# Optimization experiments

Measured on AMD Instinct MI355X. Metric: run time of the kernel, lower is better.

## Reference

```python
import jax, jax.numpy as jnp
import numpy as np

B, S, I, C, N, V, O = 32, 256, 256, 512, 1024, 64, 256
EPS = 1e-12


def setup_inputs() -> dict:
    key = jax.random.key(0)
    ks = iter(jax.random.split(key, 40))

    def rn(shape, scale=0.05):
        return (jax.random.normal(next(ks), shape, jnp.float32) * scale)

    inp = {
        'x': jax.random.normal(next(ks), (B, S, I), jnp.float32),
        # LSTM controller (PyTorch gate order i,f,g,o)
        'lstm_Wih': rn((4 * C, I + V)), 'lstm_Whh': rn((4 * C, C)),
        'lstm_bih': rn((4 * C,)), 'lstm_bhh': rn((4 * C,)),
        # read head
        'r_key_W': rn((V, C)), 'r_key_b': rn((V,)),
        'r_str_W': rn((1, C)), 'r_str_b': rn((1,)),
        'r_gate_W': rn((1, C)), 'r_gate_b': rn((1,)),
        'r_shift_W': rn((3, C)), 'r_shift_b': rn((3,)),
        'r_gamma_W': rn((1, C)), 'r_gamma_b': rn((1,)),
        # write head (uses its own key/strength layers, plus erase/add)
        'w_key_W': rn((V, C)), 'w_key_b': rn((V,)),
        'w_str_W': rn((1, C)), 'w_str_b': rn((1,)),
        'w_erase_W': rn((V, C)), 'w_erase_b': rn((V,)),
        'w_add_W': rn((V, C)), 'w_add_b': rn((V,)),
        # output projection
        'out_W': rn((O, C + V)), 'out_b': rn((O,)),
    }
    return inp


def _lin(x, W, b):
    return x @ W.T + b


def _normalize(x, axis):
    n = jnp.linalg.norm(x, axis=axis, keepdims=True)
    return x / jnp.maximum(n, EPS)


def _content_addressing(key_vec, memory, strength):
    # key_vec: [B,V], memory: [B,N,V], strength: [B,1]
    kn = _normalize(key_vec, 1)
    mn = _normalize(memory, 2)
    sim = jnp.einsum('bv,bnv->bn', kn, mn)
    return jax.nn.softmax(strength * sim, axis=1)


def _ntm_forward(x, lstm_Wih, lstm_Whh, lstm_bih, lstm_bhh,
                 r_key_W, r_key_b, r_str_W, r_str_b, r_gate_W, r_gate_b,
                 r_shift_W, r_shift_b, r_gamma_W, r_gamma_b,
                 w_key_W, w_key_b, w_str_W, w_str_b,
                 w_erase_W, w_erase_b, w_add_W, w_add_b, out_W, out_b):
    b = x.shape[0]
    h0 = jnp.zeros((b, C), x.dtype)
    c0 = jnp.zeros((b, C), x.dtype)
    mem0 = jnp.zeros((b, N, V), x.dtype)
    rv0 = jnp.zeros((b, V), x.dtype)

    def step(carry, xt):
        h, c, memory, read_vec = carry
        # LSTM cell
        ci = jnp.concatenate([xt, read_vec], axis=1)          # [B, I+V]
        gates = _lin(ci, lstm_Wih, lstm_bih) + _lin(h, lstm_Whh, lstm_bhh)
        ig, fg, gg, og = jnp.split(gates, 4, axis=1)
        c = jax.nn.sigmoid(fg) * c + jax.nn.sigmoid(ig) * jnp.tanh(gg)
        h = jax.nn.sigmoid(og) * jnp.tanh(c)

        # read head
        key_r = jnp.tanh(_lin(h, r_key_W, r_key_b))
        str_r = jax.nn.softplus(_lin(h, r_str_W, r_str_b))
        gate = jax.nn.sigmoid(_lin(h, r_gate_W, r_gate_b))
        _shift = jax.nn.softmax(_lin(h, r_shift_W, r_shift_b), axis=1)  # computed but unused (as in source)
        gamma = 1.0 + jax.nn.softplus(_lin(h, r_gamma_W, r_gamma_b))
        cw = _content_addressing(key_r, memory, str_r)        # [B,N]
        sharp = cw ** gamma
        lw = sharp / jnp.sum(sharp, axis=1, keepdims=True)
        fw = gate * lw + (1.0 - gate) * cw
        read_vec = jnp.einsum('bn,bnv->bv', fw, memory)

        # write head (erase then add)
        key_w = jnp.tanh(_lin(h, w_key_W, w_key_b))
        str_w = jax.nn.softplus(_lin(h, w_str_W, w_str_b))
        ww = _content_addressing(key_w, memory, str_w)        # [B,N]
        erase = jax.nn.sigmoid(_lin(h, w_erase_W, w_erase_b))  # [B,V]
        add = jnp.tanh(_lin(h, w_add_W, w_add_b))              # [B,V]
        memory = memory * (1.0 - ww[:, :, None] * erase[:, None, :]) \
                 + ww[:, :, None] * add[:, None, :]

        out = _lin(jnp.concatenate([h, read_vec], axis=1), out_W, out_b)
        return (h, c, memory, read_vec), out

    (_, _, final_memory, _), outs = jax.lax.scan(
        step, (h0, c0, mem0, rv0), jnp.swapaxes(x, 0, 1))
    return jnp.swapaxes(outs, 0, 1), final_memory


def reference(x, lstm_Wih, lstm_Whh, lstm_bih, lstm_bhh,
              r_key_W, r_key_b, r_str_W, r_str_b, r_gate_W, r_gate_b,
              r_shift_W, r_shift_b, r_gamma_W, r_gamma_b,
              w_key_W, w_key_b, w_str_W, w_str_b,
              w_erase_W, w_erase_b, w_add_W, w_add_b, out_W, out_b):
    return _ntm_forward(x, lstm_Wih, lstm_Whh, lstm_bih, lstm_bhh,
                        r_key_W, r_key_b, r_str_W, r_str_b, r_gate_W, r_gate_b,
                        r_shift_W, r_shift_b, r_gamma_W, r_gamma_b,
                        w_key_W, w_key_b, w_str_W, w_str_b,
                        w_erase_W, w_erase_b, w_add_W, w_add_b, out_W, out_b)
```

## Files before the change

### kernel.cpp

```cpp
#include <hip/hip_runtime.h>

#define Bv 32
#define Sv 256
#define Iv 256
#define Cv 512
#define Nv 1024
#define Vv 64
#define Ov 256
#define NBLK 256
#define NTHR 256

#define CLAIM_I(x)   ((x)*8)
#define GAL_I(x,q)   (64 + ((x)*4+(q))*8)
#define XROOT_I(x)   (320 + (x)*8)
#define PB_I(x,b)    (384 + ((x)*4+(b))*8)
#define ZERO_BYTES   (640*4)
#define FBASE 1024
#define HBU(x,t1,bb)  (FBASE + (x)*2048 + (t1)*1024 + (bb)*256)
#define RVPU(x,bb,k)  (FBASE + 16384 + (x)*1024 + (bb)*256 + (k)*32)
#define SUMPF(x,bb,k) (FBASE + 24576 + (x)*128 + (bb)*32 + (k)*4)
#define HDSF(x,bb)    (FBASE + 25600 + ((x)*4+(bb))*260)

struct KP {
  const float *x, *Wih, *Whh, *bih, *bhh;
  const float *rkW, *rkb, *rsW, *rsb, *rgW, *rgb, *rgammaW, *rgammab;
  const float *wkW, *wkb, *wsW, *wsb, *weW, *web, *waW, *wab;
  const float *outW, *outb;
  float *out;
  float *memout;
  float *ws;
};

typedef _Float16 half2v __attribute__((ext_vector_type(2)));
union HU { unsigned u; half2v h; };

__device__ inline float sigf(float x){ return 1.f/(1.f+expf(-x)); }
__device__ inline float softplusf(float x){ return fmaxf(x,0.f) + log1pf(expf(-fabsf(x))); }
__device__ inline unsigned packh(float a, float b){
  HU z; z.h = half2v{(_Float16)a, (_Float16)b}; return z.u;
}
__device__ inline float h2lo(unsigned u){ HU z; z.u = u; return (float)z.h.x; }
__device__ inline float h2hi(unsigned u){ HU z; z.u = u; return (float)z.h.y; }
__device__ inline float dot2(unsigned w, unsigned a, float acc){
  HU wu, au; wu.u = w; au.u = a;
  return __builtin_amdgcn_fdot2(wu.h, au.h, acc, false);
}

__device__ inline void stg_f(float* p, float v){
  asm volatile("global_store_dword %0, %1, off sc0" :: "v"(p), "v"(v) : "memory");
}
__device__ inline void stg_u(unsigned* p, unsigned v){
  asm volatile("global_store_dword %0, %1, off sc0" :: "v"(p), "v"(v) : "memory");
}
#define LDG4U(dst, addr) asm volatile("global_load_dwordx4 %0, %1, off sc0" : "=v"(dst) : "v"(addr) : "memory")
#define LDG4F(dst, addr) asm volatile("global_load_dwordx4 %0, %1, off sc0" : "=v"(dst) : "v"(addr) : "memory")
#define LDGU(dst, addr)  asm volatile("global_load_dword %0, %1, off sc0"  : "=v"(dst) : "v"(addr) : "memory")
#define WAITV do { asm volatile("s_waitcnt vmcnt(0)" ::: "memory"); __builtin_amdgcn_sched_barrier(0); } while(0)

#define AADD(p,v) __hip_atomic_fetch_add((p),(v),__ATOMIC_RELAXED,__HIP_MEMORY_SCOPE_AGENT)
#define ALD(p)    __hip_atomic_load((p),__ATOMIC_RELAXED,__HIP_MEMORY_SCOPE_AGENT)

#define SPIN(cond_expr) do { unsigned sp = 0; \
  while (cond_expr){ __builtin_amdgcn_s_sleep(2); \
    if (((++sp)&1023u)==0u && (__builtin_amdgcn_s_memrealtime()-t0) > 300000000ULL) break; } } while(0)

__device__ inline float headact(int o, float s){
  if (o < 64)  return tanhf(s);
  if (o == 64) return softplusf(s);
  if (o == 65) return sigf(s);
  if (o == 66) return 1.f + softplusf(s);
  if (o < 131) return tanhf(s);
  if (o == 131) return softplusf(s);
  if (o < 196) return sigf(s);
  return tanhf(s);
}
__device__ inline void head_src(const KP& P, int o, const float** row, float* bias){
  if (o < 64)       { *row = P.rkW + o*Cv;        *bias = P.rkb[o]; }
  else if (o == 64) { *row = P.rsW;               *bias = P.rsb[0]; }
  else if (o == 65) { *row = P.rgW;               *bias = P.rgb[0]; }
  else if (o == 66) { *row = P.rgammaW;           *bias = P.rgammab[0]; }
  else if (o < 131) { *row = P.wkW + (o-67)*Cv;   *bias = P.wkb[o-67]; }
  else if (o == 131){ *row = P.wsW;               *bias = P.wsb[0]; }
  else if (o < 196) { *row = P.weW + (o-132)*Cv;  *bias = P.web[o-132]; }
  else              { *row = P.waW + (o-196)*Cv;  *bias = P.wab[o-196]; }
}

__global__ __launch_bounds__(NTHR) void ntm_kernel(KP P){
  __shared__ unsigned Wg[64][420];
  __shared__ unsigned actL[4][420];
  __shared__ float memL[128][66];
  __shared__ float gb[64][4];
  __shared__ float biasL[64];
  __shared__ float htmpf[16][5];
  __shared__ unsigned hOwnL[256];
  __shared__ float headsL[264];
  __shared__ float knr[64], knw[64];
  __shared__ float scal[8];
  __shared__ float fwL[128], wwL[128];
  __shared__ float red[32][9];
  __shared__ float red2[2][4];
  __shared__ float sumred[8][4];
  __shared__ float rvpartL[4][64];
  __shared__ float rvfin[64];
  __shared__ int sXcd, sRank;

  const int tid = threadIdx.x;
  float* wsf = P.ws;
  unsigned* wsu = (unsigned*)P.ws;
  int* wsi = (int*)P.ws;
  const unsigned long long t0 = __builtin_amdgcn_s_memrealtime();

  if (tid == 0){
    unsigned xcc;
    asm volatile("s_getreg_b32 %0, hwreg(20, 0, 32)" : "=s"(xcc));
    int xc = (int)(xcc & 7u);
    int rk = AADD(&wsi[CLAIM_I(xc)], 1);
    sXcd = xc; sRank = rk & 31;
  }
  __syncthreads();
  const int xcd = sXcd, rank = sRank;
  const int bl_own = rank >> 3;
  const int rk8 = rank & 7;
  const int bglob = xcd*4 + bl_own;
  const int obase = (rk8 < 4) ? rk8*33 : 132 + (rk8-4)*32;

  for (int idx = tid; idx < 64*416; idx += NTHR){
    int rl = idx / 416, u = idx % 416;
    int gr = (rl>>4)*Cv + rank*16 + (rl&15);
    int c0 = 2*u;
    float a, b2;
    if (c0 < 320){ a = P.Wih[gr*320 + c0]; b2 = P.Wih[gr*320 + c0 + 1]; }
    else { int q = c0 - 320; a = P.Whh[gr*512 + q]; b2 = P.Whh[gr*512 + q + 1]; }
    Wg[rl][u] = packh(a, b2);
  }
  if (tid < 64){
    int gr = (tid>>4)*Cv + rank*16 + (tid&15);
    biasL[tid] = P.bih[gr] + P.bhh[gr];
  }
  for (int idx = tid; idx < 128*66; idx += NTHR) ((float*)memL)[idx] = 0.f;
  __syncthreads();

  float cS = 0.f;
  float er = 0.f, eg = 0.f, ew = 0.f;
  int gs = 0, pbs = 0;

  for (int t = 0; t < Sv; ++t){
    {
      int bb = tid>>6, part = tid&63;
      const float* xp = P.x + ((size_t)(xcd*4+bb)*Sv + (size_t)t)*Iv + part*4;
      float4 xv = *(const float4*)xp;
      actL[bb][part*2]   = packh(xv.x, xv.y);
      actL[bb][part*2+1] = packh(xv.z, xv.w);
      if (t > 0){
        uint4 hq;
        LDG4U(hq, wsu + HBU(xcd,(t+1)&1,bb) + part*4);
        unsigned q0=0,q1=0,q2=0,q3=0,q4=0,q5=0,q6=0,q7=0;
        int b2 = tid>>5, uix = tid&31;
        if (tid < 128){
          const unsigned* rb = wsu + RVPU(xcd,b2,0) + uix;
          LDGU(q0, rb+0*32); LDGU(q1, rb+1*32); LDGU(q2, rb+2*32); LDGU(q3, rb+3*32);
          LDGU(q4, rb+4*32); LDGU(q5, rb+5*32); LDGU(q6, rb+6*32); LDGU(q7, rb+7*32);
        }
        WAITV;
        *(uint4*)&actL[bb][160 + part*4] = hq;
        if (tid < 128){
          float lo = h2lo(q0)+h2lo(q1)+h2lo(q2)+h2lo(q3)+h2lo(q4)+h2lo(q5)+h2lo(q6)+h2lo(q7);
          float hi = h2hi(q0)+h2hi(q1)+h2hi(q2)+h2hi(q3)+h2hi(q4)+h2hi(q5)+h2hi(q6)+h2hi(q7);
          actL[b2][128+uix] = packh(lo, hi);
        }
      } else {
        for (int idx = tid; idx < 4*288; idx += NTHR){
          int bb2 = idx/288, u = 128 + idx%288;
          actL[bb2][u] = 0u;
        }
      }
    }
    __syncthreads();
    {
      int g = tid>>6, l = tid&63, rr = l>>2, bb = l&3, row = g*16+rr;
      const unsigned* wr = &Wg[row][0];
      const unsigned* ar = &actL[bb][0];
      float a0 = biasL[row], a1 = 0.f, a2 = 0.f, a3 = 0.f;
      #pragma unroll 13
      for (int u = 0; u < 416; u += 8){
        uint4 w0 = *(const uint4*)(wr+u);
        uint4 v0 = *(const uint4*)(ar+u);
        uint4 w1 = *(const uint4*)(wr+u+4);
        uint4 v1 = *(const uint4*)(ar+u+4);
        a0 = dot2(w0.x, v0.x, a0); a1 = dot2(w0.y, v0.y, a1);
        a2 = dot2(w0.z, v0.z, a2); a3 = dot2(w0.w, v0.w, a3);
        a0 = dot2(w1.x, v1.x, a0); a1 = dot2(w1.y, v1.y, a1);
        a2 = dot2(w1.z, v1.z, a2); a3 = dot2(w1.w, v1.w, a3);
      }
      gb[row][bb] = (a0+a1)+(a2+a3);
    }
    __syncthreads();
    if (tid < 64){
      int j = tid>>2, bb = tid&3;
      float ig = gb[j][bb], fg = gb[16+j][bb], gg = gb[32+j][bb], og = gb[48+j][bb];
      cS = sigf(fg)*cS + sigf(ig)*tanhf(gg);
      htmpf[j][bb] = sigf(og)*tanhf(cS);
    }
    __syncthreads();
    if (tid < 32){
      int pr = tid>>2, bb = tid&3;
      stg_u(wsu + HBU(xcd,t&1,bb) + rank*8 + pr, packh(htmpf[2*pr][bb], htmpf[2*pr+1][bb]));
    }
    WAITV;
    __syncthreads();
    if (tid == 0){
      int a = AADD(&wsi[GAL_I(xcd, rank>>3)], 1);
      if (a == 8*(gs+1) - 1) AADD(&wsi[XROOT_I(xcd)], 1);
    }
    if (t > 0){
      int oo = tid>>3, kc = tid&7;
      int o = rk8*32 + oo;
      const float* wrow = P.outW + o*576 + kc*72;
      const unsigned* ab = &actL[bl_own][0];
      float p = 0.f;
      if (kc < 7){
        int u0 = 160 + kc*36;
        #pragma unroll 9
        for (int i = 0; i < 36; ++i){
          unsigned u = ab[u0+i];
          p += h2lo(u)*wrow[2*i] + h2hi(u)*wrow[2*i+1];
        }
      } else {
        #pragma unroll
        for (int i = 0; i < 4; ++i){
          unsigned u = ab[412+i];
          p += h2lo(u)*wrow[2*i] + h2hi(u)*wrow[2*i+1];
        }
        #pragma unroll 8
        for (int i = 0; i < 32; ++i){
          unsigned u = ab[128+i];
          p += h2lo(u)*wrow[8+2*i] + h2hi(u)*wrow[9+2*i];
        }
      }
      red[oo][kc] = p;
      __syncthreads();
      if (tid < 32){
        int o2 = rk8*32 + tid;
        float s = P.outb[o2];
        #pragma unroll
        for (int k2 = 0; k2 < 8; ++k2) s += red[tid][k2];
        P.out[((size_t)bglob*Sv + (t-1))*Ov + o2] = s;
      }
    }
    if (tid == 0){ SPIN(ALD(&wsi[XROOT_I(xcd)]) < 4*(gs+1)); }
    __syncthreads();
    ++gs;

    if (tid < 64){
      uint4 hq;
      LDG4U(hq, wsu + HBU(xcd,t&1,bl_own) + tid*4);
      WAITV;
      *(uint4*)&hOwnL[tid*4] = hq;
    }
    __syncthreads();
    {
      int oo = tid>>3, kc = tid&7;
      int o = obase + oo;
      const float* row; float bias;
      head_src(P, o, &row, &bias);
      float p = 0.f;
      #pragma unroll 8
      for (int i = 0; i < 32; ++i){
        unsigned u = hOwnL[kc*32 + i];
        p += h2lo(u)*row[kc*64 + 2*i] + h2hi(u)*row[kc*64 + 2*i + 1];
      }
      red[oo][kc] = p;
    }
    __syncthreads();
    if (tid < 32){
      int o = obase + tid;
      const float* row; float bias;
      head_src(P, o, &row, &bias);
      float s = bias;
      #pragma unroll
      for (int k2 = 0; k2 < 8; ++k2) s += red[tid][k2];
      stg_f(wsf + HDSF(xcd,bl_own) + o, headact(o, s));
    }
    if (rk8 < 4 && tid < 64){
      int o = obase + 32;
      const float* row; float bias;
      head_src(P, o, &row, &bias);
      float p = 0.f;
      #pragma unroll
      for (int i = 0; i < 4; ++i){
        unsigned u = hOwnL[tid*4 + i];
        p += h2lo(u)*row[tid*8 + 2*i] + h2hi(u)*row[tid*8 + 2*i + 1];
      }
      #pragma unroll
      for (int off = 32; off; off >>= 1) p += __shfl_xor(p, off);
      if (tid == 0) stg_f(wsf + HDSF(xcd,bl_own) + o, headact(o, bias + p));
    }
    WAITV;
    __syncthreads();
    if (tid == 0){
      AADD(&wsi[PB_I(xcd,bl_own)], 1);
      SPIN(ALD(&wsi[PB_I(xcd,bl_own)]) < 8*(pbs+1));
    }
    __syncthreads();
    ++pbs;

    if (tid < 65){
      float4 hv;
      LDG4F(hv, wsf + HDSF(xcd,bl_own) + tid*4);
      WAITV;
      *(float4*)&headsL[tid*4] = hv;
    }
    __syncthreads();
    if (tid < 64){
      float kr = headsL[tid], kw = headsL[67+tid];
      float sr = kr*kr, sw2 = kw*kw;
      #pragma unroll
      for (int off = 32; off; off >>= 1){ sr += __shfl_xor(sr, off); sw2 += __shfl_xor(sw2, off); }
      knr[tid] = kr * (1.f/fmaxf(sqrtf(sr), 1e-12f));
      knw[tid] = kw * (1.f/fmaxf(sqrtf(sw2), 1e-12f));
    }
    __syncthreads();
    er = 0.f; eg = 0.f; ew = 0.f;
    {
      float str_r = headsL[64], gamma = headsL[66], str_w = headsL[131];
      if (tid < 128){
        float dr = 0.f, dw = 0.f, nn = 0.f;
        #pragma unroll 8
        for (int v = 0; v < 64; ++v){
          float m = memL[tid][v];
          dr += m*knr[v]; dw += m*knw[v]; nn += m*m;
        }
        float innm = 1.f/fmaxf(sqrtf(nn), 1e-12f);
        float tr = str_r*(dr*innm - 1.f);
        er = expf(tr);
        eg = expf(gamma*tr);
        ew = expf(str_w*(dw*innm - 1.f));
      }
      float s0 = er, s1 = eg, s2 = ew;
      #pragma unroll
      for (int off = 32; off; off >>= 1){
        s0 += __shfl_xor(s0, off); s1 += __shfl_xor(s1, off); s2 += __shfl_xor(s2, off);
      }
      if ((tid & 63) == 0 && tid < 128){
        int wv = tid>>6; red2[wv][0] = s0; red2[wv][1] = s1; red2[wv][2] = s2;
      }
      __syncthreads();
      if (tid == 0){
        float* sp = wsf + SUMPF(xcd,bl_own,rk8);
        stg_f(sp+0, red2[0][0]+red2[1][0]);
        stg_f(sp+1, red2[0][1]+red2[1][1]);
        stg_f(sp+2, red2[0][2]+red2[1][2]);
      }
    }
    WAITV;
    __syncthreads();
    if (tid == 0){
      AADD(&wsi[PB_I(xcd,bl_own)], 1);
      SPIN(ALD(&wsi[PB_I(xcd,bl_own)]) < 8*(pbs+1));
    }
    __syncthreads();
    ++pbs;

    if (tid < 8){
      float4 sv;
      LDG4F(sv, wsf + SUMPF(xcd,bl_own,tid));
      WAITV;
      *(float4*)&sumred[tid][0] = sv;
    }
    __syncthreads();
    if (tid == 0){
      float Se=0.f, Sg=0.f, Sw=0.f;
      #pragma unroll
      for (int k2 = 0; k2 < 8; ++k2){ Se += sumred[k2][0]; Sg += sumred[k2][1]; Sw += sumred[k2][2]; }
      scal[4]=Se; scal[5]=Sg; scal[6]=Sw;
    }
    __syncthreads();
    if (tid < 128){
      float gate_s = headsL[65];
      fwL[tid] = gate_s*(eg/scal[5]) + (1.f - gate_s)*(er/scal[4]);
      wwL[tid] = ew/scal[6];
    }
    __syncthreads();
    {
      int v = tid & 63, cc = tid >> 6;
      float p = 0.f;
      #pragma unroll 8
      for (int j = 0; j < 32; ++j){ int r = cc*32 + j; p += fwL[r]*memL[r][v]; }
      rvpartL[cc][v] = p;
    }
    __syncthreads();
    if (tid < 64) rvfin[tid] = rvpartL[0][tid]+rvpartL[1][tid]+rvpartL[2][tid]+rvpartL[3][tid];
    __syncthreads();
    if (tid < 32)
      stg_u(wsu + RVPU(xcd,bl_own,rk8) + tid, packh(rvfin[2*tid], rvfin[2*tid+1]));
    WAITV;
    __syncthreads();
    if (tid == 0){
      int a = AADD(&wsi[GAL_I(xcd, rank>>3)], 1);
      if (a == 8*(gs+1) - 1) AADD(&wsi[XROOT_I(xcd)], 1);
    }
    #pragma unroll 4
    for (int e2 = 0; e2 < 32; ++e2){
      int flat = tid + e2*256;
      int r = flat >> 6, v2 = flat & 63;
      memL[r][v2] = memL[r][v2]*(1.f - wwL[r]*headsL[132+v2]) + wwL[r]*headsL[196+v2];
    }
    if (tid == 0){ SPIN(ALD(&wsi[XROOT_I(xcd)]) < 4*(gs+1)); }
    __syncthreads();
    ++gs;
  }

  {
    int bb = tid>>6, part = tid&63;
    uint4 hq;
    LDG4U(hq, wsu + HBU(xcd,(Sv-1)&1,bb) + part*4);
    unsigned q0=0,q1=0,q2=0,q3=0,q4=0,q5=0,q6=0,q7=0;
    int b2 = tid>>5, uix = tid&31;
    if (tid < 128){
      const unsigned* rb = wsu + RVPU(xcd,b2,0) + uix;
      LDGU(q0, rb+0*32); LDGU(q1, rb+1*32); LDGU(q2, rb+2*32); LDGU(q3, rb+3*32);
      LDGU(q4, rb+4*32); LDGU(q5, rb+5*32); LDGU(q6, rb+6*32); LDGU(q7, rb+7*32);
    }
    WAITV;
    *(uint4*)&actL[bb][160 + part*4] = hq;
    if (tid < 128){
      float lo = h2lo(q0)+h2lo(q1)+h2lo(q2)+h2lo(q3)+h2lo(q4)+h2lo(q5)+h2lo(q6)+h2lo(q7);
      float hi = h2hi(q0)+h2hi(q1)+h2hi(q2)+h2hi(q3)+h2hi(q4)+h2hi(q5)+h2hi(q6)+h2hi(q7);
      actL[b2][128+uix] = packh(lo, hi);
    }
  }
  __syncthreads();
  {
    int oo = tid>>3, kc = tid&7;
    int o = rk8*32 + oo;
    const float* wrow = P.outW + o*576 + kc*72;
    const unsigned* ab = &actL[bl_own][0];
    float p = 0.f;
    if (kc < 7){
      int u0 = 160 + kc*36;
      #pragma unroll 9
      for (int i = 0; i < 36; ++i){
        unsigned u = ab[u0+i];
        p += h2lo(u)*wrow[2*i] + h2hi(u)*wrow[2*i+1];
      }
    } else {
      #pragma unroll
      for (int i = 0; i < 4; ++i){
        unsigned u = ab[412+i];
        p += h2lo(u)*wrow[2*i] + h2hi(u)*wrow[2*i+1];
      }
      #pragma unroll 8
      for (int i = 0; i < 32; ++i){
        unsigned u = ab[128+i];
        p += h2lo(u)*wrow[8+2*i] + h2hi(u)*wrow[9+2*i];
      }
    }
    red[oo][kc] = p;
    __syncthreads();
    if (tid < 32){
      int o2 = rk8*32 + tid;
      float s = P.outb[o2];
      #pragma unroll
      for (int k2 = 0; k2 < 8; ++k2) s += red[tid][k2];
      P.out[((size_t)bglob*Sv + (Sv-1))*Ov + o2] = s;
    }
  }
  for (int e2 = 0; e2 < 32; ++e2){
    int flat = tid + e2*256;
    int r = flat >> 6, v2 = flat & 63;
    P.memout[((size_t)bglob*Nv + (size_t)rk8*128 + r)*Vv + v2] = memL[r][v2];
  }
}

extern "C" void kernel_launch(void* const* d_in, const int* in_sizes, int n_in,
                              void* d_out, int out_size, void* d_ws, size_t ws_size,
                              hipStream_t stream) {
  (void)in_sizes; (void)n_in; (void)out_size; (void)ws_size;
  KP p;
  p.x       = (const float*)d_in[0];
  p.Wih     = (const float*)d_in[1];
  p.Whh     = (const float*)d_in[2];
  p.bih     = (const float*)d_in[3];
  p.bhh     = (const float*)d_in[4];
  p.rkW     = (const float*)d_in[5];  p.rkb     = (const float*)d_in[6];
  p.rsW     = (const float*)d_in[7];  p.rsb     = (const float*)d_in[8];
  p.rgW     = (const float*)d_in[9];  p.rgb     = (const float*)d_in[10];
  p.rgammaW = (const float*)d_in[13]; p.rgammab = (const float*)d_in[14];
  p.wkW     = (const float*)d_in[15]; p.wkb     = (const float*)d_in[16];
  p.wsW     = (const float*)d_in[17]; p.wsb     = (const float*)d_in[18];
  p.weW     = (const float*)d_in[19]; p.web     = (const float*)d_in[20];
  p.waW     = (const float*)d_in[21]; p.wab     = (const float*)d_in[22];
  p.outW    = (const float*)d_in[23]; p.outb    = (const float*)d_in[24];
  p.out     = (float*)d_out;
  p.memout  = (float*)d_out + (size_t)Bv*Sv*Ov;
  p.ws      = (float*)d_ws;

  hipMemsetAsync(d_ws, 0, ZERO_BYTES, stream);
  hipLaunchKernelGGL(ntm_kernel, dim3(NBLK), dim3(NTHR), 0, stream, p);
}
```

Baseline: 4.942 ms.

## Remove softmax-sum barrier by deferring normalization into next step's read combine

Each block now writes unnormalized read partials (separate content and gamma-sharpened vectors) plus exp sums, and drops the per-step cross-block barrier that waited for the softmax denominators. Normalization and the gate blend are applied when the next timestep gathers the partials, and the write-weight sum is read after the existing gather barrier, before the memory update. This removes one grid-level spin synchronization per timestep, at the cost of doubled partial traffic, extra local barriers, and fp16 storage of unnormalized sums, which risks precision loss. The spin sleep interval is also lengthened.

```diff
diff --git a/kernel.cpp b/kernel.cpp
--- a/kernel.cpp
+++ b/kernel.cpp
@@ -17,9 +17,9 @@
 #define ZERO_BYTES   (640*4)
 #define FBASE 1024
 #define HBU(x,t1,bb)  (FBASE + (x)*2048 + (t1)*1024 + (bb)*256)
-#define RVPU(x,bb,k)  (FBASE + 16384 + (x)*1024 + (bb)*256 + (k)*32)
-#define SUMPF(x,bb,k) (FBASE + 24576 + (x)*128 + (bb)*32 + (k)*4)
-#define HDSF(x,bb)    (FBASE + 25600 + ((x)*4+(bb))*260)
+#define EGU(x,bb,k)   (FBASE + 16384 + (x)*2048 + (bb)*512 + (k)*64)
+#define SUMPF(x,bb,k) (FBASE + 32768 + (x)*128 + (bb)*32 + (k)*4)
+#define HDSF(x,bb)    (FBASE + 33792 + ((x)*4+(bb))*260)
 
 struct KP {
   const float *x, *Wih, *Whh, *bih, *bhh;
@@ -55,13 +55,14 @@
 #define LDG4U(dst, addr) asm volatile("global_load_dwordx4 %0, %1, off sc0" : "=v"(dst) : "v"(addr) : "memory")
 #define LDG4F(dst, addr) asm volatile("global_load_dwordx4 %0, %1, off sc0" : "=v"(dst) : "v"(addr) : "memory")
 #define LDGU(dst, addr)  asm volatile("global_load_dword %0, %1, off sc0"  : "=v"(dst) : "v"(addr) : "memory")
+#define LDGF(dst, addr)  asm volatile("global_load_dword %0, %1, off sc0"  : "=v"(dst) : "v"(addr) : "memory")
 #define WAITV do { asm volatile("s_waitcnt vmcnt(0)" ::: "memory"); __builtin_amdgcn_sched_barrier(0); } while(0)
 
 #define AADD(p,v) __hip_atomic_fetch_add((p),(v),__ATOMIC_RELAXED,__HIP_MEMORY_SCOPE_AGENT)
 #define ALD(p)    __hip_atomic_load((p),__ATOMIC_RELAXED,__HIP_MEMORY_SCOPE_AGENT)
 
 #define SPIN(cond_expr) do { unsigned sp = 0; \
-  while (cond_expr){ __builtin_amdgcn_s_sleep(2); \
+  while (cond_expr){ __builtin_amdgcn_s_sleep(8); \
     if (((++sp)&1023u)==0u && (__builtin_amdgcn_s_memrealtime()-t0) > 300000000ULL) break; } } while(0)
 
 __device__ inline float headact(int o, float s){
@@ -96,12 +97,14 @@
   __shared__ float headsL[264];
   __shared__ float knr[64], knw[64];
   __shared__ float scal[8];
-  __shared__ float fwL[128], wwL[128];
+  __shared__ float erL2[128], egL2[128], ewL[128];
   __shared__ float red[32][9];
   __shared__ float red2[2][4];
-  __shared__ float sumred[8][4];
-  __shared__ float rvpartL[4][64];
-  __shared__ float rvfin[64];
+  __shared__ float sumS1[4][8][4];
+  __shared__ float gLld[4], cEL[4], cGL[4];
+  __shared__ float sumS4[8][4];
+  __shared__ float rvpE[4][64], rvpG[4][64];
+  __shared__ float rvfinE[64], rvfinG[64];
   __shared__ int sXcd, sRank;
 
   const int tid = threadIdx.x;
@@ -141,7 +144,6 @@
   __syncthreads();
 
   float cS = 0.f;
-  float er = 0.f, eg = 0.f, ew = 0.f;
   int gs = 0, pbs = 0;
 
   for (int t = 0; t < Sv; ++t){
@@ -153,20 +155,40 @@
       actL[bb][part*2+1] = packh(xv.z, xv.w);
       if (t > 0){
         uint4 hq;
+        unsigned e0,e1,e2,e3,e4,e5,e6,e7,g0,g1,g2,g3,g4,g5,g6,g7;
+        float4 sv = {0,0,0,0}; float gval = 0.f;
+        int b2 = tid>>5, j = tid&31;
         LDG4U(hq, wsu + HBU(xcd,(t+1)&1,bb) + part*4);
-        unsigned q0=0,q1=0,q2=0,q3=0,q4=0,q5=0,q6=0,q7=0;
-        int b2 = tid>>5, uix = tid&31;
         if (tid < 128){
-          const unsigned* rb = wsu + RVPU(xcd,b2,0) + uix;
-          LDGU(q0, rb+0*32); LDGU(q1, rb+1*32); LDGU(q2, rb+2*32); LDGU(q3, rb+3*32);
-          LDGU(q4, rb+4*32); LDGU(q5, rb+5*32); LDGU(q6, rb+6*32); LDGU(q7, rb+7*32);
-        }
+          const unsigned* eb = wsu + EGU(xcd,b2,0) + j;
+          LDGU(e0,eb+0*64); LDGU(e1,eb+1*64); LDGU(e2,eb+2*64); LDGU(e3,eb+3*64);
+          LDGU(e4,eb+4*64); LDGU(e5,eb+5*64); LDGU(e6,eb+6*64); LDGU(e7,eb+7*64);
+          const unsigned* ggb = eb + 32;
+          LDGU(g0,ggb+0*64); LDGU(g1,ggb+1*64); LDGU(g2,ggb+2*64); LDGU(g3,ggb+3*64);
+          LDGU(g4,ggb+4*64); LDGU(g5,ggb+5*64); LDGU(g6,ggb+6*64); LDGU(g7,ggb+7*64);
+        }
+        if (tid < 32){ LDG4F(sv, wsf + SUMPF(xcd, tid>>3, tid&7)); }
+        if (tid >= 32 && tid < 36){ LDGF(gval, wsf + HDSF(xcd, tid-32) + 65); }
         WAITV;
         *(uint4*)&actL[bb][160 + part*4] = hq;
+        if (tid < 32) *(float4*)&sumS1[tid>>3][tid&7][0] = sv;
+        if (tid >= 32 && tid < 36) gLld[tid-32] = gval;
+        __syncthreads();
+        if (tid < 4){
+          float Se = 0.f, Sg = 0.f;
+          #pragma unroll
+          for (int k2 = 0; k2 < 8; ++k2){ Se += sumS1[tid][k2][0]; Sg += sumS1[tid][k2][1]; }
+          float g = gLld[tid];
+          cEL[tid] = (1.f - g)/Se;
+          cGL[tid] = g/Sg;
+        }
+        __syncthreads();
         if (tid < 128){
-          float lo = h2lo(q0)+h2lo(q1)+h2lo(q2)+h2lo(q3)+h2lo(q4)+h2lo(q5)+h2lo(q6)+h2lo(q7);
-          float hi = h2hi(q0)+h2hi(q1)+h2hi(q2)+h2hi(q3)+h2hi(q4)+h2hi(q5)+h2hi(q6)+h2hi(q7);
-          actL[b2][128+uix] = packh(lo, hi);
+          float Elo = h2lo(e0)+h2lo(e1)+h2lo(e2)+h2lo(e3)+h2lo(e4)+h2lo(e5)+h2lo(e6)+h2lo(e7);
+          float Ehi = h2hi(e0)+h2hi(e1)+h2hi(e2)+h2hi(e3)+h2hi(e4)+h2hi(e5)+h2hi(e6)+h2hi(e7);
+          float Glo = h2lo(g0)+h2lo(g1)+h2lo(g2)+h2lo(g3)+h2lo(g4)+h2lo(g5)+h2lo(g6)+h2lo(g7);
+          float Ghi = h2hi(g0)+h2hi(g1)+h2hi(g2)+h2hi(g3)+h2hi(g4)+h2hi(g5)+h2hi(g6)+h2hi(g7);
+          actL[b2][128 + j] = packh(cGL[b2]*Glo + cEL[b2]*Elo, cGL[b2]*Ghi + cEL[b2]*Ehi);
         }
       } else {
         for (int idx = tid; idx < 4*288; idx += NTHR){
@@ -304,11 +326,11 @@
     __syncthreads();
     ++pbs;
 
-    if (tid < 65){
-      float4 hv;
-      LDG4F(hv, wsf + HDSF(xcd,bl_own) + tid*4);
+    {
+      float4 hv = {0,0,0,0};
+      if (tid < 65){ LDG4F(hv, wsf + HDSF(xcd,bl_own) + tid*4); }
       WAITV;
-      *(float4*)&headsL[tid*4] = hv;
+      if (tid < 65){ *(float4*)&headsL[tid*4] = hv; }
     }
     __syncthreads();
     if (tid < 64){
@@ -320,9 +342,9 @@
       knw[tid] = kw * (1.f/fmaxf(sqrtf(sw2), 1e-12f));
     }
     __syncthreads();
-    er = 0.f; eg = 0.f; ew = 0.f;
     {
       float str_r = headsL[64], gamma = headsL[66], str_w = headsL[131];
+      float er = 0.f, eg = 0.f, ew = 0.f;
       if (tid < 128){
         float dr = 0.f, dw = 0.f, nn = 0.f;
         #pragma unroll 8
@@ -335,6 +357,7 @@
         er = expf(tr);
         eg = expf(gamma*tr);
         ew = expf(str_w*(dw*innm - 1.f));
+        erL2[tid] = er; egL2[tid] = eg; ewL[tid] = ew;
       }
       float s0 = er, s1 = eg, s2 = ew;
       #pragma unroll
@@ -352,81 +375,101 @@
         stg_f(sp+2, red2[0][2]+red2[1][2]);
       }
     }
-    WAITV;
-    __syncthreads();
-    if (tid == 0){
-      AADD(&wsi[PB_I(xcd,bl_own)], 1);
-      SPIN(ALD(&wsi[PB_I(xcd,bl_own)]) < 8*(pbs+1));
-    }
-    __syncthreads();
-    ++pbs;
-
-    if (tid < 8){
-      float4 sv;
-      LDG4F(sv, wsf + SUMPF(xcd,bl_own,tid));
-      WAITV;
-      *(float4*)&sumred[tid][0] = sv;
-    }
-    __syncthreads();
-    if (tid == 0){
-      float Se=0.f, Sg=0.f, Sw=0.f;
-      #pragma unroll
-      for (int k2 = 0; k2 < 8; ++k2){ Se += sumred[k2][0]; Sg += sumred[k2][1]; Sw += sumred[k2][2]; }
-      scal[4]=Se; scal[5]=Sg; scal[6]=Sw;
-    }
-    __syncthreads();
-    if (tid < 128){
-      float gate_s = headsL[65];
-      fwL[tid] = gate_s*(eg/scal[5]) + (1.f - gate_s)*(er/scal[4]);
-      wwL[tid] = ew/scal[6];
-    }
-    __syncthreads();
     {
       int v = tid & 63, cc = tid >> 6;
-      float p = 0.f;
+      float pE = 0.f, pG = 0.f;
       #pragma unroll 8
-      for (int j = 0; j < 32; ++j){ int r = cc*32 + j; p += fwL[r]*memL[r][v]; }
-      rvpartL[cc][v] = p;
-    }
-    __syncthreads();
-    if (tid < 64) rvfin[tid] = rvpartL[0][tid]+rvpartL[1][tid]+rvpartL[2][tid]+rvpartL[3][tid];
+      for (int j = 0; j < 32; ++j){
+        int r = cc*32 + j;
+        float m = memL[r][v];
+        pE += erL2[r]*m; pG += egL2[r]*m;
+      }
+      rvpE[cc][v] = pE; rvpG[cc][v] = pG;
+    }
+    __syncthreads();
+    if (tid < 64){
+      rvfinE[tid] = rvpE[0][tid]+rvpE[1][tid]+rvpE[2][tid]+rvpE[3][tid];
+      rvfinG[tid] = rvpG[0][tid]+rvpG[1][tid]+rvpG[2][tid]+rvpG[3][tid];
+    }
     __syncthreads();
     if (tid < 32)
-      stg_u(wsu + RVPU(xcd,bl_own,rk8) + tid, packh(rvfin[2*tid], rvfin[2*tid+1]));
+      stg_u(wsu + EGU(xcd,bl_own,rk8) + tid, packh(rvfinE[2*tid], rvfinE[2*tid+1]));
+    else if (tid < 64)
+      stg_u(wsu + EGU(xcd,bl_own,rk8) + tid, packh(rvfinG[2*(tid-32)], rvfinG[2*(tid-32)+1]));
     WAITV;
     __syncthreads();
     if (tid == 0){
       int a = AADD(&wsi[GAL_I(xcd, rank>>3)], 1);
       if (a == 8*(gs+1) - 1) AADD(&wsi[XROOT_I(xcd)], 1);
-    }
-    #pragma unroll 4
-    for (int e2 = 0; e2 < 32; ++e2){
-      int flat = tid + e2*256;
-      int r = flat >> 6, v2 = flat & 63;
-      memL[r][v2] = memL[r][v2]*(1.f - wwL[r]*headsL[132+v2]) + wwL[r]*headsL[196+v2];
-    }
-    if (tid == 0){ SPIN(ALD(&wsi[XROOT_I(xcd)]) < 4*(gs+1)); }
+      SPIN(ALD(&wsi[XROOT_I(xcd)]) < 4*(gs+1));
+    }
     __syncthreads();
     ++gs;
+
+    {
+      float4 sv = {0,0,0,0};
+      if (tid < 8){ LDG4F(sv, wsf + SUMPF(xcd,bl_own,tid)); }
+      WAITV;
+      if (tid < 8){ *(float4*)&sumS4[tid][0] = sv; }
+    }
+    __syncthreads();
+    if (tid == 0){
+      float Sw = 0.f;
+      #pragma unroll
+      for (int k2 = 0; k2 < 8; ++k2) Sw += sumS4[k2][2];
+      scal[6] = Sw;
+    }
+    __syncthreads();
+    {
+      float rSw = 1.f/scal[6];
+      #pragma unroll 4
+      for (int e2 = 0; e2 < 32; ++e2){
+        int flat = tid + e2*256;
+        int r = flat >> 6, v2 = flat & 63;
+        float ww = ewL[r]*rSw;
+        memL[r][v2] = memL[r][v2]*(1.f - ww*headsL[132+v2]) + ww*headsL[196+v2];
+      }
+    }
+    __syncthreads();
   }
 
   {
     int bb = tid>>6, part = tid&63;
     uint4 hq;
+    unsigned e0,e1,e2,e3,e4,e5,e6,e7,g0,g1,g2,g3,g4,g5,g6,g7;
+    float4 sv = {0,0,0,0}; float gval = 0.f;
+    int b2 = tid>>5, j = tid&31;
     LDG4U(hq, wsu + HBU(xcd,(Sv-1)&1,bb) + part*4);
-    unsigned q0=0,q1=0,q2=0,q3=0,q4=0,q5=0,q6=0,q7=0;
-    int b2 = tid>>5, uix = tid&31;
     if (tid < 128){
-      const unsigned* rb = wsu + RVPU(xcd,b2,0) + uix;
-      LDGU(q0, rb+0*32); LDGU(q1, rb+1*32); LDGU(q2, rb+2*32); LDGU(q3, rb+3*32);
-      LDGU(q4, rb+4*32); LDGU(q5, rb+5*32); LDGU(q6, rb+6*32); LDGU(q7, rb+7*32);
-    }
+      const unsigned* eb = wsu + EGU(xcd,b2,0) + j;
+      LDGU(e0,eb+0*64); LDGU(e1,eb+1*64); LDGU(e2,eb+2*64); LDGU(e3,eb+3*64);
+      LDGU(e4,eb+4*64); LDGU(e5,eb+5*64); LDGU(e6,eb+6*64); LDGU(e7,eb+7*64);
+      const unsigned* ggb = eb + 32;
+      LDGU(g0,ggb+0*64); LDGU(g1,ggb+1*64); LDGU(g2,ggb+2*64); LDGU(g3,ggb+3*64);
+      LDGU(g4,ggb+4*64); LDGU(g5,ggb+5*64); LDGU(g6,ggb+6*64); LDGU(g7,ggb+7*64);
+    }
+    if (tid < 32){ LDG4F(sv, wsf + SUMPF(xcd, tid>>3, tid&7)); }
+    if (tid >= 32 && tid < 36){ LDGF(gval, wsf + HDSF(xcd, tid-32) + 65); }
     WAITV;
     *(uint4*)&actL[bb][160 + part*4] = hq;
+    if (tid < 32) *(float4*)&sumS1[tid>>3][tid&7][0] = sv;
+    if (tid >= 32 && tid < 36) gLld[tid-32] = gval;
+    __syncthreads();
+    if (tid < 4){
+      float Se = 0.f, Sg = 0.f;
+      #pragma unroll
+      for (int k2 = 0; k2 < 8; ++k2){ Se += sumS1[tid][k2][0]; Sg += sumS1[tid][k2][1]; }
+      float g = gLld[tid];
+      cEL[tid] = (1.f - g)/Se;
+      cGL[tid] = g/Sg;
+    }
+    __syncthreads();
     if (tid < 128){
-      float lo = h2lo(q0)+h2lo(q1)+h2lo(q2)+h2lo(q3)+h2lo(q4)+h2lo(q5)+h2lo(q6)+h2lo(q7);
-      float hi = h2hi(q0)+h2hi(q1)+h2hi(q2)+h2hi(q3)+h2hi(q4)+h2hi(q5)+h2hi(q6)+h2hi(q7);
-      actL[b2][128+uix] = packh(lo, hi);
+      float Elo = h2lo(e0)+h2lo(e1)+h2lo(e2)+h2lo(e3)+h2lo(e4)+h2lo(e5)+h2lo(e6)+h2lo(e7);
+      float Ehi = h2hi(e0)+h2hi(e1)+h2hi(e2)+h2hi(e3)+h2hi(e4)+h2hi(e5)+h2hi(e6)+h2hi(e7);
+      float Glo = h2lo(g0)+h2lo(g1)+h2lo(g2)+h2lo(g3)+h2lo(g4)+h2lo(g5)+h2lo(g6)+h2lo(g7);
+      float Ghi = h2hi(g0)+h2hi(g1)+h2hi(g2)+h2hi(g3)+h2hi(g4)+h2hi(g5)+h2hi(g6)+h2hi(g7);
+      actL[b2][128 + j] = packh(cGL[b2]*Glo + cEL[b2]*Elo, cGL[b2]*Ghi + cEL[b2]*Ehi);
     }
   }
   __syncthreads();
```

After: 5.105 ms. 1.03x slower.
